# Performance work log

Hardware: AMD Instinct MI355X
Metric: run time of the kernel (lower is better)

Reference implementation:

```python
import jax, jax.numpy as jnp
import numpy as np

B, N, T, F_IN, H, OUT = 64, 207, 48, 6, 64, 1
RANK = 24  # fixed inner dim of learned adjacency factors


def setup_inputs() -> dict:
    key = jax.random.key(0)
    ks = jax.random.split(key, 10)
    s = lambda k, shp, sc=1.0: jax.random.normal(k, shp, jnp.float32) * sc
    return {
        "x": s(ks[0], (B, N, T, F_IN)),
        "N1": s(ks[1], (N, RANK)),
        "N2": s(ks[2], (RANK, N)),
        "W1": s(ks[3], (F_IN, H), 0.2),
        "b1": jnp.zeros((H,), jnp.float32),
        "W2": s(ks[4], (H, H), 0.1),
        "b2": jnp.zeros((H,), jnp.float32),
        "W_ih": s(ks[5], (4 * H, H), 0.1),
        "W_hh": s(ks[6], (4 * H, H), 0.1),
        "b_ih": jnp.zeros((4 * H,), jnp.float32),
        "b_hh": jnp.zeros((4 * H,), jnp.float32),
        "W_fc": s(ks[7], (H, OUT), 0.1),
        "b_fc": jnp.zeros((OUT,), jnp.float32),
    }


def reference(x, N1, N2, W1, b1, W2, b2, W_ih, W_hh, b_ih, b_hh, W_fc, b_fc):
    Bn, Nn, Tn, Fn = x.shape
    # sigmoid(N1@N2) > 0 everywhere -> dense_to_sparse yields ALL N^2 edges
    # (self-loops included); GCNConv's gcn_norm adds one extra self-loop,
    # edge weights all 1 -> A = ones + I, deg = N+1, symmetric normalization.
    adj = jax.nn.sigmoid(N1 @ N2)
    mask = (adj > 0).astype(x.dtype)  # structurally all-ones
    A = mask + jnp.eye(Nn, dtype=x.dtype)
    dinv = jax.lax.rsqrt(A.sum(axis=1))
    A_hat = dinv[:, None] * A * dinv[None, :]  # [N, N]

    xt = jnp.transpose(x, (0, 2, 1, 3))  # [B, T, N, F]
    # GCNConv: propagate(x @ W) with sym-norm, then bias; relu; dropout=eval no-op
    h = jax.nn.relu(jnp.einsum('mn,btnh->btmh', A_hat, xt @ W1) + b1)
    h = jax.nn.relu(jnp.einsum('mn,btnh->btmh', A_hat, h @ W2) + b2)

    # [B, T, N, H] -> [B*N, T, H] for the LSTM
    seq = jnp.transpose(h, (0, 2, 1, 3)).reshape(Bn * Nn, Tn, -1)
    Hd = W_hh.shape[1]

    def step(carry, x_t):
        h_prev, c_prev = carry
        g = x_t @ W_ih.T + b_ih + h_prev @ W_hh.T + b_hh
        i, f, gg, o = jnp.split(g, 4, axis=-1)  # torch gate order i,f,g,o
        c = jax.nn.sigmoid(f) * c_prev + jax.nn.sigmoid(i) * jnp.tanh(gg)
        h_new = jax.nn.sigmoid(o) * jnp.tanh(c)
        return (h_new, c), None

    h0 = jnp.zeros((Bn * Nn, Hd), x.dtype)
    (hT, _), _ = jax.lax.scan(step, (h0, h0), jnp.transpose(seq, (1, 0, 2)))
    out = hT @ W_fc + b_fc  # [B*N, OUT]
    return out.reshape(Bn, Nn, -1)
```

## Files before the change

### kernel.cpp

```cpp
#include <hip/hip_runtime.h>
#include <math.h>

#define NB 64
#define NN 207
#define NT 48
#define NF 6
#define NH 64
#define NSEQ (NB*NN)
#define NG   (NSEQ/16)
#define TSU  ((size_t)NSEQ*NH)

typedef short bf8_t __attribute__((ext_vector_type(8)));
typedef float f4_t  __attribute__((ext_vector_type(4)));
typedef unsigned short ushort;
typedef unsigned int uint;

__device__ __forceinline__ ushort bf16h(float x){
  uint u = __float_as_uint(x);
  return (ushort)((u + 0x7FFF + ((u>>16)&1)) >> 16);
}
__device__ __forceinline__ float bf16f(ushort h){
  return __uint_as_float((uint)h << 16);
}
__device__ __forceinline__ float fsig(float x){
  return __builtin_amdgcn_rcpf(1.0f + __expf(-x));
}
__device__ __forceinline__ float ftanh(float x){
  x = fminf(15.0f, fmaxf(-15.0f, x));
  float e = __expf(2.0f*x);
  return 1.0f - 2.0f*__builtin_amdgcn_rcpf(e + 1.0f);
}


#define HW 72
#define XS6 40
#define GCN7_LDS_BYTES (208*HW*2 + (207*XS6 + NF*64 + 64 + 64 + 6*64 + 6*64 + 48)*4)

__global__ __launch_bounds__(256, 2) void gcn_kernel(
    const float* __restrict__ x, const float* __restrict__ W1, const float* __restrict__ b1,
    const float* __restrict__ W2, const float* __restrict__ b2,
    ushort* __restrict__ sxh, ushort* __restrict__ sxl)
{
  extern __shared__ char smraw[];
  ushort* h1b = (ushort*)smraw;
  float*  xs6 = (float*)(h1b + 208*HW);
  float*  W1s = xs6 + 207*XS6;
  float*  b1s = W1s + NF*64;
  float*  b2s = b1s + 64;
  float*  S2_ = b2s + 64;
  float*  r1_ = S2_ + 6*64;
  float*  xsA = r1_ + 6*64;

  const int tid = threadIdx.x;
  const int tg = blockIdx.x, b = blockIdx.y;
  const float inv = 1.0f/208.0f;
  const int l = tid & 63;
  const int w = __builtin_amdgcn_readfirstlane(tid >> 6);
  const int col = l & 15, q = l >> 4;
  const int cw = w*16 + col;

  for (int i=tid; i<6*64; i+=256){ S2_[i]=0.f; r1_[i]=0.f; }
  if (tid < 48) xsA[tid] = 0.f;
  if (tid < 72) h1b[207*HW + tid] = 0;

  for (int i=tid;i<NF*64;i+=256) W1s[i]=W1[i];
  if (tid<64){ b1s[tid]=b1[tid]; b2s[tid]=b2[tid]; }
  {
    const float* xb = x + (size_t)b*NN*(NT*NF) + (size_t)tg*36;
    for (int i=tid; i<207*9; i+=256){
      int n = i/9, c = (i - n*9)*4;
      *(float4*)&xs6[n*XS6 + c] = *(const float4*)&xb[(size_t)n*(NT*NF) + c];
    }
  }
  __syncthreads();

  if (tid < 144){
    int tt = tid/24, rem = tid - tt*24, f = rem>>2, p = rem&3;
    float ps = 0.f;
    for (int n=p; n<NN; n+=4) ps += xs6[n*XS6 + tt*6 + f];
    atomicAdd(&xsA[tt*8+f], ps);
  }

  float wtmp[16];
  #pragma unroll
  for (int kc=0;kc<2;kc++)
    #pragma unroll
    for (int j=0;j<8;j++)
      wtmp[kc*8+j] = W2[(size_t)(kc*32 + q*8 + j)*64 + cw];
  bf8_t B2[2];
  #pragma unroll
  for (int kc=0;kc<2;kc++){
    bf8_t ph;
    #pragma unroll
    for (int j=0;j<8;j++) ph[j] = (short)bf16h(wtmp[kc*8+j]);
    B2[kc]=ph;
  }
  __syncthreads();

  const int ht4 = (tid & 15) * 4;
  const int nti = tid >> 4;

  #pragma unroll 1
  for (int tt=0; tt<6; tt++){
    const int t = tg*6 + tt;
    {
      float s1v[4];
      #pragma unroll
      for (int j=0;j<4;j++){
        float a = 0.f;
        #pragma unroll
        for (int f=0;f<NF;f++) a += xsA[tt*8+f]*W1s[f*64 + ht4 + j];
        s1v[j] = a;
      }
      float cs0=0.f, cs1=0.f, cs2=0.f, cs3=0.f;
      #pragma unroll 1
      for (int p=0;p<4;p++){
        int nt = p*16 + nti;
        if (nt < 52){
          #pragma unroll
          for (int i=0;i<4;i++){
            int n = 4*nt+i;
            if (n < NN){
              float a0=0.f,a1=0.f,a2=0.f,a3=0.f;
              #pragma unroll
              for (int f=0;f<NF;f++){
                float xv = xs6[n*XS6 + tt*6 + f];
                float4 wv = *(const float4*)&W1s[f*64 + ht4];
                a0+=xv*wv.x; a1+=xv*wv.y; a2+=xv*wv.z; a3+=xv*wv.w;
              }
              float v0=(a0+s1v[0])*inv + b1s[ht4+0]; v0 = v0>0.f?v0:0.f;
              float v1=(a1+s1v[1])*inv + b1s[ht4+1]; v1 = v1>0.f?v1:0.f;
              float v2=(a2+s1v[2])*inv + b1s[ht4+2]; v2 = v2>0.f?v2:0.f;
              float v3=(a3+s1v[3])*inv + b1s[ht4+3]; v3 = v3>0.f?v3:0.f;
              ushort4 hi;
              hi.x=bf16h(v0); hi.y=bf16h(v1); hi.z=bf16h(v2); hi.w=bf16h(v3);
              *(ushort4*)&h1b[n*HW + ht4] = hi;
              cs0+=v0; cs1+=v1; cs2+=v2; cs3+=v3;
            }
          }
        }
      }
      atomicAdd(&r1_[tt*64+ht4+0], cs0);
      atomicAdd(&r1_[tt*64+ht4+1], cs1);
      atomicAdd(&r1_[tt*64+ht4+2], cs2);
      atomicAdd(&r1_[tt*64+ht4+3], cs3);
    }
    __syncthreads();

    {
      int h = tid & 63, pp = tid >> 6;
      float ps = 0.f;
      #pragma unroll
      for (int k=0;k<16;k++) ps += r1_[tt*64+pp*16+k]*W2[(size_t)(pp*16+k)*64 + h];
      atomicAdd(&S2_[tt*64+h], ps);
    }

    f4_t acc[13];
    #pragma unroll
    for (int mt=0;mt<13;mt++){ f4_t z; z[0]=0.f;z[1]=0.f;z[2]=0.f;z[3]=0.f; acc[mt]=z; }
    #pragma unroll 2
    for (int mt=0;mt<13;mt++){
      #pragma unroll
      for (int kc=0;kc<2;kc++){
        bf8_t ah = *(const bf8_t*)(h1b + (mt*16+col)*HW + kc*32 + q*8);
        acc[mt] = __builtin_amdgcn_mfma_f32_16x16x32_bf16(ah, B2[kc], acc[mt], 0,0,0);
      }
    }
    __syncthreads();

    {
      const float s2v = S2_[tt*64+cw], b2v = b2s[cw];
      const size_t obase = (size_t)t*TSU + (size_t)(b*NN)*NH + cw;
      #pragma unroll
      for (int mt=0;mt<13;mt++){
        #pragma unroll
        for (int r=0;r<4;r++){
          int n = mt*16 + q*4 + r;
          if (n < NN){
            float v = (acc[mt][r] + s2v)*inv + b2v;
            v = v>0.f ? v : 0.f;
            ushort hb = bf16h(v);
            sxh[obase + (size_t)n*NH] = hb;
            sxl[obase + (size_t)n*NH] = bf16h(v - bf16f(hb));
          }
        }
      }
    }
  }
}

#define HS 68

__global__ __launch_bounds__(256, 1) void lstm12_kernel(
    const ushort* __restrict__ sxh, const ushort* __restrict__ sxl,
    const float* __restrict__ Wih, const float* __restrict__ Whh,
    const float* __restrict__ bih, const float* __restrict__ bhh,
    const float* __restrict__ Wfc, const float* __restrict__ bfc, float* __restrict__ out)
{
  __shared__ uint hf[2][16*HS + 4];

  const int tid = threadIdx.x;
  const int l = tid & 63;
  const int w = __builtin_amdgcn_readfirstlane(tid >> 6);
  const int col = l & 15, q = l >> 4;
  const int g = blockIdx.x;

  bf8_t Bh[4][4], Bl[4][4];
  #pragma unroll
  for (int mat=0; mat<2; mat++){
    const float* W = mat ? Whh : Wih;
    #pragma unroll
    for (int ty=0; ty<4; ty++){
      #pragma unroll
      for (int kk=0; kk<2; kk++){
        const float* wp = W + (size_t)(ty*64 + w*16 + col)*64 + kk*32 + q*8;
        bf8_t ph, pl;
        #pragma unroll
        for (int j=0;j<8;j++){
          float wv = wp[j];
          ushort hb = bf16h(wv);
          ph[j] = (short)hb;
          pl[j] = (short)bf16h(wv - bf16f(hb));
        }
        Bh[ty][mat*2+kk] = ph;
        Bl[ty][mat*2+kk] = pl;
      }
    }
  }
  float bias[4];
  #pragma unroll
  for (int ty=0;ty<4;ty++){
    int r = ty*64 + w*16 + col;
    bias[ty] = bih[r] + bhh[r];
  }
  float c[4];
  #pragma unroll
  for (int i=0;i<4;i++) c[i]=0.f;

  for (int i=tid; i<16*HS; i+=256) hf[0][i] = 0;

  const ushort* xgh = sxh + (size_t)g*1024 + (size_t)(col*64 + q*8);
  const ushort* xgl = sxl + (size_t)g*1024 + (size_t)(col*64 + q*8);

  bf8_t pxh[2][2], pxl[2][2];
  #pragma unroll
  for (int s2=0; s2<2; s2++){
    const size_t off = (size_t)s2*TSU;
    pxh[s2][0] = *(const bf8_t*)(xgh + off);
    pxh[s2][1] = *(const bf8_t*)(xgh + off + 32);
    pxl[s2][0] = *(const bf8_t*)(xgl + off);
    pxl[s2][1] = *(const bf8_t*)(xgl + off + 32);
  }

  const int d = w*16 + col;
  const uint* hrd = &hf[0][0] + col*HS + q*8;
  __syncthreads();

  #pragma unroll 2
  for (int t=0; t<NT; t++){
    const int cur = t & 1;
    bf8_t cxh0 = pxh[cur][0], cxh1 = pxh[cur][1];
    bf8_t cxl0 = pxl[cur][0], cxl1 = pxl[cur][1];
    if (t+2 < NT){
      const size_t off = (size_t)(t+2)*TSU;
      pxh[cur][0] = *(const bf8_t*)(xgh + off);
      pxh[cur][1] = *(const bf8_t*)(xgh + off + 32);
      pxl[cur][0] = *(const bf8_t*)(xgl + off);
      pxl[cur][1] = *(const bf8_t*)(xgl + off + 32);
    }

    bf8_t hh[2], hl[2];
    {
      const uint* hb = hrd + (cur ? (16*HS+4) : 0);
      uint4 h0 = *(const uint4*)(hb);
      uint4 h1 = *(const uint4*)(hb + 4);
      uint4 h2 = *(const uint4*)(hb + 32);
      uint4 h3 = *(const uint4*)(hb + 36);
      uint u[8];
      u[0]=h0.x;u[1]=h0.y;u[2]=h0.z;u[3]=h0.w;u[4]=h1.x;u[5]=h1.y;u[6]=h1.z;u[7]=h1.w;
      #pragma unroll
      for (int j=0;j<8;j++){ hh[0][j]=(short)(u[j]>>16); hl[0][j]=(short)(u[j]&0xffff); }
      u[0]=h2.x;u[1]=h2.y;u[2]=h2.z;u[3]=h2.w;u[4]=h3.x;u[5]=h3.y;u[6]=h3.z;u[7]=h3.w;
      #pragma unroll
      for (int j=0;j<8;j++){ hh[1][j]=(short)(u[j]>>16); hl[1][j]=(short)(u[j]&0xffff); }
    }

    f4_t acc[4];
    #pragma unroll
    for (int ty=0;ty<4;ty++){ f4_t z; z[0]=bias[ty];z[1]=bias[ty];z[2]=bias[ty];z[3]=bias[ty]; acc[ty]=z; }
    #pragma unroll
    for (int ty=0;ty<4;ty++){
      acc[ty] = __builtin_amdgcn_mfma_f32_16x16x32_bf16(cxh0,  Bh[ty][0], acc[ty], 0,0,0);
      acc[ty] = __builtin_amdgcn_mfma_f32_16x16x32_bf16(cxl0,  Bh[ty][0], acc[ty], 0,0,0);
      acc[ty] = __builtin_amdgcn_mfma_f32_16x16x32_bf16(cxh0,  Bl[ty][0], acc[ty], 0,0,0);
      acc[ty] = __builtin_amdgcn_mfma_f32_16x16x32_bf16(cxh1,  Bh[ty][1], acc[ty], 0,0,0);
      acc[ty] = __builtin_amdgcn_mfma_f32_16x16x32_bf16(cxl1,  Bh[ty][1], acc[ty], 0,0,0);
      acc[ty] = __builtin_amdgcn_mfma_f32_16x16x32_bf16(cxh1,  Bl[ty][1], acc[ty], 0,0,0);
      acc[ty] = __builtin_amdgcn_mfma_f32_16x16x32_bf16(hh[0], Bh[ty][2], acc[ty], 0,0,0);
      acc[ty] = __builtin_amdgcn_mfma_f32_16x16x32_bf16(hl[0], Bh[ty][2], acc[ty], 0,0,0);
      acc[ty] = __builtin_amdgcn_mfma_f32_16x16x32_bf16(hh[0], Bl[ty][2], acc[ty], 0,0,0);
      acc[ty] = __builtin_amdgcn_mfma_f32_16x16x32_bf16(hh[1], Bh[ty][3], acc[ty], 0,0,0);
      acc[ty] = __builtin_amdgcn_mfma_f32_16x16x32_bf16(hl[1], Bh[ty][3], acc[ty], 0,0,0);
      acc[ty] = __builtin_amdgcn_mfma_f32_16x16x32_bf16(hh[1], Bl[ty][3], acc[ty], 0,0,0);
    }

    {
      uint* hw = &hf[cur^1][0];
      #pragma unroll
      for (int r=0;r<4;r++){
        float ig = fsig(acc[0][r]);
        float fg = fsig(acc[1][r]);
        float gt = ftanh(acc[2][r]);
        float og = fsig(acc[3][r]);
        float cc = fg*c[r] + ig*gt;
        c[r] = cc;
        float hv = og*ftanh(cc);
        int off = (q*4+r)*HS + d;
        if (t != NT-1){
          ushort hb2 = bf16h(hv);
          ushort lb2 = bf16h(hv - bf16f(hb2));
          hw[off] = ((uint)hb2<<16) | (uint)lb2;
        } else {
          hw[off] = __float_as_uint(hv);
        }
      }
    }
    __syncthreads();
  }

  if (tid < 16){
    float a = bfc[0];
    const uint* hT = &hf[NT&1][0];
    #pragma unroll 8
    for (int k=0;k<64;k++) a += __uint_as_float(hT[tid*HS + k]) * Wfc[k];
    out[g*16 + tid] = a;
  }
}

extern "C" void kernel_launch(void* const* d_in, const int* in_sizes, int n_in,
                              void* d_out, int out_size, void* d_ws, size_t ws_size,
                              hipStream_t stream) {
  const float* x   = (const float*)d_in[0];
  const float* W1  = (const float*)d_in[3];
  const float* b1  = (const float*)d_in[4];
  const float* W2  = (const float*)d_in[5];
  const float* b2  = (const float*)d_in[6];
  const float* Wih = (const float*)d_in[7];
  const float* Whh = (const float*)d_in[8];
  const float* bih = (const float*)d_in[9];
  const float* bhh = (const float*)d_in[10];
  const float* Wfc = (const float*)d_in[11];
  const float* bfc = (const float*)d_in[12];

  ushort* sxh = (ushort*)d_ws;
  ushort* sxl = sxh + (size_t)NT*TSU;
  float*  out = (float*)d_out;

  hipFuncSetAttribute((const void*)gcn_kernel, hipFuncAttributeMaxDynamicSharedMemorySize, GCN7_LDS_BYTES);

  gcn_kernel<<<dim3(NT/6, NB), 256, GCN7_LDS_BYTES, stream>>>(x, W1, b1, W2, b2, sxh, sxl);
  lstm12_kernel<<<NG, 256, 0, stream>>>(sxh, sxl, Wih, Whh, bih, bhh, Wfc, bfc, out);
}
```

Measured before the change: 347.6 us.

## Split LSTM gate GEMM K-dimension across two wave groups with LDS reduction

The LSTM kernel moves from 256 to 512 threads per block. Each half of the waves computes the gate products over one half of the K dimension (32 of the 64 input and hidden features), and the two partial results are summed through an LDS exchange buffer. The gate nonlinearity work is then split between the wave pairs, and the h buffer becomes single-buffered. The intent is to halve the serial MFMA chain per wave in each timestep and raise occupancy. In exchange it adds an extra __syncthreads and LDS round trip on every step of the serial recurrence.

```diff
diff --git a/kernel.cpp b/kernel.cpp
--- a/kernel.cpp
+++ b/kernel.cpp
@@ -191,98 +191,84 @@
 
 #define HS 68
 
-__global__ __launch_bounds__(256, 1) void lstm12_kernel(
+__global__ __launch_bounds__(512, 3) void lstm13_kernel(
     const ushort* __restrict__ sxh, const ushort* __restrict__ sxl,
     const float* __restrict__ Wih, const float* __restrict__ Whh,
     const float* __restrict__ bih, const float* __restrict__ bhh,
     const float* __restrict__ Wfc, const float* __restrict__ bfc, float* __restrict__ out)
 {
-  __shared__ uint hf[2][16*HS + 4];
+  __shared__ uint hf[16*HS + 8];
+  __shared__ f4_t Gex[8][4][64];
 
   const int tid = threadIdx.x;
   const int l = tid & 63;
   const int w = __builtin_amdgcn_readfirstlane(tid >> 6);
+  const int wd = w & 3, wk = w >> 2;
   const int col = l & 15, q = l >> 4;
   const int g = blockIdx.x;
 
-  bf8_t Bh[4][4], Bl[4][4];
+  bf8_t Bh[4][2], Bl[4][2];
   #pragma unroll
   for (int mat=0; mat<2; mat++){
     const float* W = mat ? Whh : Wih;
     #pragma unroll
     for (int ty=0; ty<4; ty++){
-      #pragma unroll
-      for (int kk=0; kk<2; kk++){
-        const float* wp = W + (size_t)(ty*64 + w*16 + col)*64 + kk*32 + q*8;
-        bf8_t ph, pl;
-        #pragma unroll
-        for (int j=0;j<8;j++){
-          float wv = wp[j];
-          ushort hb = bf16h(wv);
-          ph[j] = (short)hb;
-          pl[j] = (short)bf16h(wv - bf16f(hb));
-        }
-        Bh[ty][mat*2+kk] = ph;
-        Bl[ty][mat*2+kk] = pl;
-      }
+      const float* wp = W + (size_t)(ty*64 + wd*16 + col)*64 + wk*32 + q*8;
+      bf8_t ph, pl;
+      #pragma unroll
+      for (int j=0;j<8;j++){
+        float wv = wp[j];
+        ushort hb = bf16h(wv);
+        ph[j] = (short)hb;
+        pl[j] = (short)bf16h(wv - bf16f(hb));
+      }
+      Bh[ty][mat] = ph;
+      Bl[ty][mat] = pl;
     }
   }
   float bias[4];
   #pragma unroll
   for (int ty=0;ty<4;ty++){
-    int r = ty*64 + w*16 + col;
-    bias[ty] = bih[r] + bhh[r];
-  }
-  float c[4];
-  #pragma unroll
-  for (int i=0;i<4;i++) c[i]=0.f;
-
-  for (int i=tid; i<16*HS; i+=256) hf[0][i] = 0;
-
-  const ushort* xgh = sxh + (size_t)g*1024 + (size_t)(col*64 + q*8);
-  const ushort* xgl = sxl + (size_t)g*1024 + (size_t)(col*64 + q*8);
-
-  bf8_t pxh[2][2], pxl[2][2];
-  #pragma unroll
-  for (int s2=0; s2<2; s2++){
-    const size_t off = (size_t)s2*TSU;
-    pxh[s2][0] = *(const bf8_t*)(xgh + off);
-    pxh[s2][1] = *(const bf8_t*)(xgh + off + 32);
-    pxl[s2][0] = *(const bf8_t*)(xgl + off);
-    pxl[s2][1] = *(const bf8_t*)(xgl + off + 32);
-  }
-
-  const int d = w*16 + col;
-  const uint* hrd = &hf[0][0] + col*HS + q*8;
+    int r = ty*64 + wd*16 + col;
+    bias[ty] = (wk==0) ? (bih[r] + bhh[r]) : 0.f;
+  }
+  float c[2];
+  c[0]=0.f; c[1]=0.f;
+
+  for (int i=tid; i<16*HS; i+=512) hf[i] = 0;
+
+  const ushort* xgh = sxh + (size_t)g*1024 + (size_t)(col*64 + wk*32 + q*8);
+  const ushort* xgl = sxl + (size_t)g*1024 + (size_t)(col*64 + wk*32 + q*8);
+
+  bf8_t pxh[2], pxl[2];
+  pxh[0] = *(const bf8_t*)(xgh);
+  pxl[0] = *(const bf8_t*)(xgl);
+  pxh[1] = *(const bf8_t*)(xgh + TSU);
+  pxl[1] = *(const bf8_t*)(xgl + TSU);
+
+  const int d = wd*16 + col;
+  const uint* hrd = &hf[0] + col*HS + wk*32 + q*8;
+  const int pw = w ^ 4;
   __syncthreads();
 
-  #pragma unroll 2
+  #pragma unroll 1
   for (int t=0; t<NT; t++){
     const int cur = t & 1;
-    bf8_t cxh0 = pxh[cur][0], cxh1 = pxh[cur][1];
-    bf8_t cxl0 = pxl[cur][0], cxl1 = pxl[cur][1];
+    bf8_t cxh = pxh[cur], cxl = pxl[cur];
     if (t+2 < NT){
       const size_t off = (size_t)(t+2)*TSU;
-      pxh[cur][0] = *(const bf8_t*)(xgh + off);
-      pxh[cur][1] = *(const bf8_t*)(xgh + off + 32);
-      pxl[cur][0] = *(const bf8_t*)(xgl + off);
-      pxl[cur][1] = *(const bf8_t*)(xgl + off + 32);
-    }
-
-    bf8_t hh[2], hl[2];
+      pxh[cur] = *(const bf8_t*)(xgh + off);
+      pxl[cur] = *(const bf8_t*)(xgl + off);
+    }
+
+    bf8_t hh, hl;
     {
-      const uint* hb = hrd + (cur ? (16*HS+4) : 0);
-      uint4 h0 = *(const uint4*)(hb);
-      uint4 h1 = *(const uint4*)(hb + 4);
-      uint4 h2 = *(const uint4*)(hb + 32);
-      uint4 h3 = *(const uint4*)(hb + 36);
+      uint4 h0 = *(const uint4*)(hrd);
+      uint4 h1 = *(const uint4*)(hrd + 4);
       uint u[8];
       u[0]=h0.x;u[1]=h0.y;u[2]=h0.z;u[3]=h0.w;u[4]=h1.x;u[5]=h1.y;u[6]=h1.z;u[7]=h1.w;
       #pragma unroll
-      for (int j=0;j<8;j++){ hh[0][j]=(short)(u[j]>>16); hl[0][j]=(short)(u[j]&0xffff); }
-      u[0]=h2.x;u[1]=h2.y;u[2]=h2.z;u[3]=h2.w;u[4]=h3.x;u[5]=h3.y;u[6]=h3.z;u[7]=h3.w;
-      #pragma unroll
-      for (int j=0;j<8;j++){ hh[1][j]=(short)(u[j]>>16); hl[1][j]=(short)(u[j]&0xffff); }
+      for (int j=0;j<8;j++){ hh[j]=(short)(u[j]>>16); hl[j]=(short)(u[j]&0xffff); }
     }
 
     f4_t acc[4];
@@ -290,39 +276,37 @@
     for (int ty=0;ty<4;ty++){ f4_t z; z[0]=bias[ty];z[1]=bias[ty];z[2]=bias[ty];z[3]=bias[ty]; acc[ty]=z; }
     #pragma unroll
     for (int ty=0;ty<4;ty++){
-      acc[ty] = __builtin_amdgcn_mfma_f32_16x16x32_bf16(cxh0,  Bh[ty][0], acc[ty], 0,0,0);
-      acc[ty] = __builtin_amdgcn_mfma_f32_16x16x32_bf16(cxl0,  Bh[ty][0], acc[ty], 0,0,0);
-      acc[ty] = __builtin_amdgcn_mfma_f32_16x16x32_bf16(cxh0,  Bl[ty][0], acc[ty], 0,0,0);
-      acc[ty] = __builtin_amdgcn_mfma_f32_16x16x32_bf16(cxh1,  Bh[ty][1], acc[ty], 0,0,0);
-      acc[ty] = __builtin_amdgcn_mfma_f32_16x16x32_bf16(cxl1,  Bh[ty][1], acc[ty], 0,0,0);
-      acc[ty] = __builtin_amdgcn_mfma_f32_16x16x32_bf16(cxh1,  Bl[ty][1], acc[ty], 0,0,0);
-      acc[ty] = __builtin_amdgcn_mfma_f32_16x16x32_bf16(hh[0], Bh[ty][2], acc[ty], 0,0,0);
-      acc[ty] = __builtin_amdgcn_mfma_f32_16x16x32_bf16(hl[0], Bh[ty][2], acc[ty], 0,0,0);
-      acc[ty] = __builtin_amdgcn_mfma_f32_16x16x32_bf16(hh[0], Bl[ty][2], acc[ty], 0,0,0);
-      acc[ty] = __builtin_amdgcn_mfma_f32_16x16x32_bf16(hh[1], Bh[ty][3], acc[ty], 0,0,0);
-      acc[ty] = __builtin_amdgcn_mfma_f32_16x16x32_bf16(hl[1], Bh[ty][3], acc[ty], 0,0,0);
-      acc[ty] = __builtin_amdgcn_mfma_f32_16x16x32_bf16(hh[1], Bl[ty][3], acc[ty], 0,0,0);
-    }
-
-    {
-      uint* hw = &hf[cur^1][0];
-      #pragma unroll
-      for (int r=0;r<4;r++){
-        float ig = fsig(acc[0][r]);
-        float fg = fsig(acc[1][r]);
-        float gt = ftanh(acc[2][r]);
-        float og = fsig(acc[3][r]);
-        float cc = fg*c[r] + ig*gt;
-        c[r] = cc;
-        float hv = og*ftanh(cc);
-        int off = (q*4+r)*HS + d;
-        if (t != NT-1){
-          ushort hb2 = bf16h(hv);
-          ushort lb2 = bf16h(hv - bf16f(hb2));
-          hw[off] = ((uint)hb2<<16) | (uint)lb2;
-        } else {
-          hw[off] = __float_as_uint(hv);
-        }
+      acc[ty] = __builtin_amdgcn_mfma_f32_16x16x32_bf16(cxh, Bh[ty][0], acc[ty], 0,0,0);
+      acc[ty] = __builtin_amdgcn_mfma_f32_16x16x32_bf16(cxl, Bh[ty][0], acc[ty], 0,0,0);
+      acc[ty] = __builtin_amdgcn_mfma_f32_16x16x32_bf16(cxh, Bl[ty][0], acc[ty], 0,0,0);
+      acc[ty] = __builtin_amdgcn_mfma_f32_16x16x32_bf16(hh,  Bh[ty][1], acc[ty], 0,0,0);
+      acc[ty] = __builtin_amdgcn_mfma_f32_16x16x32_bf16(hl,  Bh[ty][1], acc[ty], 0,0,0);
+      acc[ty] = __builtin_amdgcn_mfma_f32_16x16x32_bf16(hh,  Bl[ty][1], acc[ty], 0,0,0);
+    }
+
+    #pragma unroll
+    for (int ty=0;ty<4;ty++) Gex[w][ty][l] = acc[ty];
+    __syncthreads();
+    #pragma unroll
+    for (int ty=0;ty<4;ty++) acc[ty] += Gex[pw][ty][l];
+
+    #pragma unroll
+    for (int j=0;j<2;j++){
+      const int r = 2*wk + j;
+      float ig = fsig(acc[0][r]);
+      float fg = fsig(acc[1][r]);
+      float gt = ftanh(acc[2][r]);
+      float og = fsig(acc[3][r]);
+      float cc = fg*c[j] + ig*gt;
+      c[j] = cc;
+      float hv = og*ftanh(cc);
+      const int off = (q*4+r)*HS + d;
+      if (t != NT-1){
+        ushort hb2 = bf16h(hv);
+        ushort lb2 = bf16h(hv - bf16f(hb2));
+        hf[off] = ((uint)hb2<<16) | (uint)lb2;
+      } else {
+        hf[off] = __float_as_uint(hv);
       }
     }
     __syncthreads();
@@ -330,9 +314,8 @@
 
   if (tid < 16){
     float a = bfc[0];
-    const uint* hT = &hf[NT&1][0];
     #pragma unroll 8
-    for (int k=0;k<64;k++) a += __uint_as_float(hT[tid*HS + k]) * Wfc[k];
+    for (int k=0;k<64;k++) a += __uint_as_float(hf[tid*HS + k]) * Wfc[k];
     out[g*16 + tid] = a;
   }
 }
@@ -359,5 +342,5 @@
   hipFuncSetAttribute((const void*)gcn_kernel, hipFuncAttributeMaxDynamicSharedMemorySize, GCN7_LDS_BYTES);
 
   gcn_kernel<<<dim3(NT/6, NB), 256, GCN7_LDS_BYTES, stream>>>(x, W1, b1, W2, b2, sxh, sxl);
-  lstm12_kernel<<<NG, 256, 0, stream>>>(sxh, sxl, Wih, Whh, bih, bhh, Wfc, bfc, out);
-}
+  lstm13_kernel<<<NG, 512, 0, stream>>>(sxh, sxl, Wih, Whh, bih, bhh, Wfc, bfc, out);
+}
```

Result: slower. 953.7 us (+174.4%).
